# Kernel optimization log

Hardware: AMD Instinct MI355X
Metric: run time of the kernel (lower is better)

The kernel has to match this reference:

```python
import jax, jax.numpy as jnp
import numpy as np


def setup_inputs() -> dict:
    key = jax.random.key(0)
    k1, k2, k3, k4 = jax.random.split(key, 4)
    n, m = 4096, 1024  # n video frames, 1024-d features
    scale = 0.02
    return {
        "x": jax.random.normal(k1, (n, m), dtype=jnp.float32),
        "WQ": jax.random.normal(k2, (m, m), dtype=jnp.float32) * scale,  # torch Linear weight [out,in]
        "WK": jax.random.normal(k3, (m, m), dtype=jnp.float32) * scale,
        "WV": jax.random.normal(k4, (m, m), dtype=jnp.float32) * scale,
    }


def _quaternion_logits(q, k):
    """Hamilton-product attention logits: 4 tensors of shape [Lq, Lk]."""
    qr, qx, qy, qz = jnp.split(q, 4, axis=-1)
    kr, kx, ky, kz = jnp.split(k, 4, axis=-1)
    dot = lambda a, b: jnp.einsum('qd,kd->qk', a, b)
    r = dot(qr, kr) - dot(qx, kx) - dot(qy, ky) - dot(qz, kz)
    i = dot(qr, kx) + dot(qx, kr) + dot(qy, kz) - dot(qz, ky)
    j = dot(qr, ky) - dot(qx, kz) + dot(qy, kr) + dot(qz, kx)
    kk = dot(qr, kz) + dot(qx, ky) - dot(qy, kx) + dot(qz, kr)
    return [r, i, j, kk]


def reference(x, WQ, WK, WV):
    # QKV projections (torch Linear, no bias): y = x @ W.T
    Q = x @ WQ.T
    K = x @ WK.T
    V = x @ WV.T
    v_vals = jnp.split(V, 4, axis=-1)  # 4 chunks of depth d/4 (tensor2tensor quaternion attn)
    logits = _quaternion_logits(Q, K)
    outs = []
    w = None
    for l, v in zip(logits, v_vals):
        w = jax.nn.softmax(l, axis=-1)  # per-component softmax over keys
        outs.append(w @ v)
    y = jnp.concatenate(outs, axis=-1)  # [n, d]
    # original returns the attention weights from the last component (loop-leaked var)
    return y, w
```

## Files before the change

kernel.cpp:

```cpp
#include <hip/hip_runtime.h>
#include <cmath>

typedef __attribute__((ext_vector_type(8))) short short8;
typedef __attribute__((ext_vector_type(8))) unsigned short ushort8_t;
typedef __attribute__((ext_vector_type(8))) _Float16 half8;
typedef __attribute__((ext_vector_type(4))) float f32x4;
typedef unsigned short u16;

__device__ __forceinline__ u16 f2h(float f) {
    _Float16 h = (_Float16)f;
    return __builtin_bit_cast(u16, h);
}
__device__ __forceinline__ float h2f(u16 b) {
    return (float)__builtin_bit_cast(_Float16, b);
}

#define GLD16(g, l)                                                              \
    __builtin_amdgcn_global_load_lds(                                            \
        (const __attribute__((address_space(1))) unsigned int*)(g),              \
        (__attribute__((address_space(3))) unsigned int*)(l), 16, 0, 0)

#define MFMA_F16(a, b, c)                                                        \
    __builtin_amdgcn_mfma_f32_16x16x32_f16(                                      \
        __builtin_bit_cast(half8, (a)), __builtin_bit_cast(half8, (b)), (c), 0, 0, 0)
#define SBAR() asm volatile("s_barrier" ::: "memory")

__global__ __launch_bounds__(256) void to_h_all(
    const float* __restrict__ x, const float* __restrict__ WQ,
    const float* __restrict__ WK, const float* __restrict__ WV,
    u16* __restrict__ xh, u16* __restrict__ Wh)
{
    int bid = blockIdx.x;
    const float* src;
    u16* dst;
    int off;
    if (bid < 4096) { src = x; dst = xh; off = bid; }
    else {
        int j = bid - 4096;
        int wsel = j >> 10;
        off = j & 1023;
        src = wsel == 0 ? WQ : (wsel == 1 ? WK : WV);
        dst = Wh + (size_t)wsel * 1024 * 1024;
    }
    int idx = off * 256 + threadIdx.x;
    float4 v = reinterpret_cast<const float4*>(src)[idx];
    ushort4 h;
    h.x = f2h(v.x); h.y = f2h(v.y); h.z = f2h(v.z); h.w = f2h(v.w);
    reinterpret_cast<ushort4*>(dst)[idx] = h;
}

__global__ __launch_bounds__(512, 2) void logits8(
    const u16* __restrict__ A, const u16* __restrict__ B, const u16* __restrict__ Bneg,
    u16* __restrict__ Pbase, float* __restrict__ pmb, float* __restrict__ psb,
    int perm_all, int sign_all)
{
    constexpr int NT = 16;
    __shared__ u16 L[2][2][256 * 64];
    const int tid = threadIdx.x;
    const int l = tid & 63, w = tid >> 6;
    const int wr = w >> 2, wc = w & 3;
    const int lr = l & 15, lh = l >> 4;
    const int bid = (int)blockIdx.x;
    const int comp = bid >> 8;
    const int perm_packed = (perm_all >> (8 * comp)) & 0xFF;
    const int sign_packed = (sign_all >> (8 * comp)) & 0xFF;
    u16* P = Pbase + (size_t)comp * 4096 * 4096;
    float* pm = pmb + (size_t)comp * 4096 * 64;
    float* ps = psb + (size_t)comp * 4096 * 64;
    const int inner = bid & 255;
    const int xcd = inner & 7, idx = inner >> 3;
    const int rowp = (xcd >> 1) * 4 + (idx >> 3);
    const int colp = (xcd & 1) * 8 + (idx & 7);
    const int row0 = rowp * 256, col0 = colp * 256;
    const int srow = l >> 3;
    const int scol = ((l & 7) ^ (l >> 3)) * 8;

    f32x4 acc[8][4] = {};

    auto stage = [&](int t) {
        int kA = t * 64;
        int ch = kA >> 8;
        int p = (perm_packed >> (2 * ch)) & 3;
        const u16* Bsrc = ((sign_packed >> ch) & 1) ? Bneg : B;
        int kB = (p << 8) + (kA & 255);
        int bf = t & 1;
        #pragma unroll
        for (int i = 0; i < 4; ++i) {
            int r0 = w * 32 + i * 8;
            GLD16(&A[(size_t)(row0 + r0 + srow) * 1024 + kA + scol], &L[bf][0][r0 * 64]);
        }
        #pragma unroll
        for (int i = 0; i < 4; ++i) {
            int r0 = w * 32 + i * 8;
            GLD16(&Bsrc[(size_t)(col0 + r0 + srow) * 1024 + kB + scol], &L[bf][1][r0 * 64]);
        }
    };
    auto readA = [&](int bf, int m, int kh) -> short8 {
        int row = wr * 128 + m * 16 + lr;
        int c = ((kh * 4 + lh) ^ (lr & 7)) * 8;
        return *reinterpret_cast<const short8*>(&L[bf][0][row * 64 + c]);
    };
    auto readB = [&](int bf, int n, int kh) -> short8 {
        int row = wc * 64 + n * 16 + lr;
        int c = ((kh * 4 + lh) ^ (lr & 7)) * 8;
        return *reinterpret_cast<const short8*>(&L[bf][1][row * 64 + c]);
    };

    stage(0);
    stage(1);
    asm volatile("s_waitcnt vmcnt(8)" ::: "memory");
    SBAR();

    #pragma unroll 2
    for (int t = 0; t < NT; ++t) {
        const int bf = t & 1;
        short8 am[4][2], bn[4][2];
        #pragma unroll
        for (int m = 0; m < 4; ++m) { am[m][0] = readA(bf, m, 0); am[m][1] = readA(bf, m, 1); }
        #pragma unroll
        for (int n = 0; n < 2; ++n) { bn[n][0] = readB(bf, n, 0); bn[n][1] = readB(bf, n, 1); }
        SBAR();
        __builtin_amdgcn_s_setprio(1);
        #pragma unroll
        for (int m = 0; m < 4; ++m)
            #pragma unroll
            for (int n = 0; n < 2; ++n) {
                acc[m][n] = MFMA_F16(am[m][0], bn[n][0], acc[m][n]);
                acc[m][n] = MFMA_F16(am[m][1], bn[n][1], acc[m][n]);
            }
        __builtin_amdgcn_s_setprio(0);
        SBAR();
        #pragma unroll
        for (int n = 2; n < 4; ++n) { bn[n][0] = readB(bf, n, 0); bn[n][1] = readB(bf, n, 1); }
        SBAR();
        __builtin_amdgcn_s_setprio(1);
        #pragma unroll
        for (int m = 0; m < 4; ++m)
            #pragma unroll
            for (int n = 2; n < 4; ++n) {
                acc[m][n] = MFMA_F16(am[m][0], bn[n][0], acc[m][n]);
                acc[m][n] = MFMA_F16(am[m][1], bn[n][1], acc[m][n]);
            }
        __builtin_amdgcn_s_setprio(0);
        SBAR();
        #pragma unroll
        for (int m = 0; m < 4; ++m) { am[m][0] = readA(bf, 4 + m, 0); am[m][1] = readA(bf, 4 + m, 1); }
        SBAR();
        __builtin_amdgcn_s_setprio(1);
        #pragma unroll
        for (int m = 0; m < 4; ++m)
            #pragma unroll
            for (int n = 2; n < 4; ++n) {
                acc[4 + m][n] = MFMA_F16(am[m][0], bn[n][0], acc[4 + m][n]);
                acc[4 + m][n] = MFMA_F16(am[m][1], bn[n][1], acc[4 + m][n]);
            }
        __builtin_amdgcn_s_setprio(0);
        SBAR();
        if (t + 2 < NT) stage(t + 2);
        SBAR();
        __builtin_amdgcn_s_setprio(1);
        #pragma unroll
        for (int m = 0; m < 4; ++m)
            #pragma unroll
            for (int n = 0; n < 2; ++n) {
                acc[4 + m][n] = MFMA_F16(am[m][0], bn[n][0], acc[4 + m][n]);
                acc[4 + m][n] = MFMA_F16(am[m][1], bn[n][1], acc[4 + m][n]);
            }
        __builtin_amdgcn_s_setprio(0);
        if (t + 2 < NT) { asm volatile("s_waitcnt vmcnt(8)" ::: "memory"); }
        else           { asm volatile("s_waitcnt vmcnt(0)" ::: "memory"); }
        SBAR();
    }

    const int tcol = (col0 >> 6) + wc;
    float* T = reinterpret_cast<float*>(&L[0][0][0]) + w * 1088;
    const int rq = l >> 2;
    const int cq = l & 3;
    #pragma unroll
    for (int m = 0; m < 8; ++m) {
        #pragma unroll
        for (int n = 0; n < 4; ++n)
            #pragma unroll
            for (int j = 0; j < 4; ++j)
                T[(lh * 4 + j) * 68 + n * 16 + lr] = acc[m][n][j];
        float vals[16];
        #pragma unroll
        for (int q = 0; q < 4; ++q) {
            f32x4 v4 = *reinterpret_cast<const f32x4*>(&T[rq * 68 + cq * 16 + q * 4]);
            vals[q * 4 + 0] = v4[0]; vals[q * 4 + 1] = v4[1];
            vals[q * 4 + 2] = v4[2]; vals[q * 4 + 3] = v4[3];
        }
        float mx = vals[0];
        #pragma unroll
        for (int c = 1; c < 16; ++c) mx = fmaxf(mx, vals[c]);
        mx = fmaxf(mx, __shfl_xor(mx, 1, 64));
        mx = fmaxf(mx, __shfl_xor(mx, 2, 64));
        float e[16];
        float s = 0.f;
        #pragma unroll
        for (int c = 0; c < 16; ++c) { e[c] = expf(vals[c] - mx); s += e[c]; }
        s += __shfl_xor(s, 1, 64);
        s += __shfl_xor(s, 2, 64);
        int row = row0 + wr * 128 + m * 16 + rq;
        if (cq == 0) {
            pm[(size_t)row * 64 + tcol] = mx;
            ps[(size_t)row * 64 + tcol] = s;
        }
        ushort8_t d0, d1;
        #pragma unroll
        for (int c = 0; c < 8; ++c) d0[c] = f2h(e[c]);
        #pragma unroll
        for (int c = 0; c < 8; ++c) d1[c] = f2h(e[c + 8]);
        size_t go = (size_t)row * 4096 + col0 + wc * 64 + cq * 16;
        *reinterpret_cast<ushort8_t*>(&P[go]) = d0;
        *reinterpret_cast<ushort8_t*>(&P[go + 8]) = d1;
    }
}

__global__ __launch_bounds__(512, 2) void qkv8(
    const u16* __restrict__ A, const u16* __restrict__ B,
    u16* __restrict__ Qh, u16* __restrict__ Kh, u16* __restrict__ Khn,
    u16* __restrict__ Vt)
{
    constexpr int NT = 16;
    __shared__ u16 L[2][2][256 * 64];
    const int tid = threadIdx.x;
    const int l = tid & 63, w = tid >> 6;
    const int wr = w >> 2, wc = w & 3;
    const int lr = l & 15, lh = l >> 4;
    const int bid = (int)blockIdx.x;
    const int wgid = (bid & 7) * 24 + (bid >> 3);
    const int row0 = (wgid / 12) * 256, col0 = (wgid % 12) * 256;
    const int srow = l >> 3;
    const int scol = ((l & 7) ^ (l >> 3)) * 8;

    f32x4 acc[8][4] = {};

    auto stage = [&](int t) {
        int k0 = t * 64;
        int bf = t & 1;
        #pragma unroll
        for (int i = 0; i < 4; ++i) {
            int r0 = w * 32 + i * 8;
            GLD16(&A[(size_t)(row0 + r0 + srow) * 1024 + k0 + scol], &L[bf][0][r0 * 64]);
        }
        #pragma unroll
        for (int i = 0; i < 4; ++i) {
            int r0 = w * 32 + i * 8;
            GLD16(&B[(size_t)(col0 + r0 + srow) * 1024 + k0 + scol], &L[bf][1][r0 * 64]);
        }
    };
    auto readA = [&](int bf, int m, int kh) -> short8 {
        int row = wr * 128 + m * 16 + lr;
        int c = ((kh * 4 + lh) ^ (lr & 7)) * 8;
        return *reinterpret_cast<const short8*>(&L[bf][0][row * 64 + c]);
    };
    auto readB = [&](int bf, int n, int kh) -> short8 {
        int row = wc * 64 + n * 16 + lr;
        int c = ((kh * 4 + lh) ^ (lr & 7)) * 8;
        return *reinterpret_cast<const short8*>(&L[bf][1][row * 64 + c]);
    };

    stage(0);
    stage(1);
    asm volatile("s_waitcnt vmcnt(8)" ::: "memory");
    SBAR();

    #pragma unroll 2
    for (int t = 0; t < NT; ++t) {
        const int bf = t & 1;
        short8 am[4][2], bn[4][2];
        #pragma unroll
        for (int m = 0; m < 4; ++m) { am[m][0] = readA(bf, m, 0); am[m][1] = readA(bf, m, 1); }
        #pragma unroll
        for (int n = 0; n < 2; ++n) { bn[n][0] = readB(bf, n, 0); bn[n][1] = readB(bf, n, 1); }
        SBAR();
        __builtin_amdgcn_s_setprio(1);
        #pragma unroll
        for (int m = 0; m < 4; ++m)
            #pragma unroll
            for (int n = 0; n < 2; ++n) {
                acc[m][n] = MFMA_F16(am[m][0], bn[n][0], acc[m][n]);
                acc[m][n] = MFMA_F16(am[m][1], bn[n][1], acc[m][n]);
            }
        __builtin_amdgcn_s_setprio(0);
        SBAR();
        #pragma unroll
        for (int n = 2; n < 4; ++n) { bn[n][0] = readB(bf, n, 0); bn[n][1] = readB(bf, n, 1); }
        SBAR();
        __builtin_amdgcn_s_setprio(1);
        #pragma unroll
        for (int m = 0; m < 4; ++m)
            #pragma unroll
            for (int n = 2; n < 4; ++n) {
                acc[m][n] = MFMA_F16(am[m][0], bn[n][0], acc[m][n]);
                acc[m][n] = MFMA_F16(am[m][1], bn[n][1], acc[m][n]);
            }
        __builtin_amdgcn_s_setprio(0);
        SBAR();
        #pragma unroll
        for (int m = 0; m < 4; ++m) { am[m][0] = readA(bf, 4 + m, 0); am[m][1] = readA(bf, 4 + m, 1); }
        SBAR();
        __builtin_amdgcn_s_setprio(1);
        #pragma unroll
        for (int m = 0; m < 4; ++m)
            #pragma unroll
            for (int n = 2; n < 4; ++n) {
                acc[4 + m][n] = MFMA_F16(am[m][0], bn[n][0], acc[4 + m][n]);
                acc[4 + m][n] = MFMA_F16(am[m][1], bn[n][1], acc[4 + m][n]);
            }
        __builtin_amdgcn_s_setprio(0);
        SBAR();
        if (t + 2 < NT) stage(t + 2);
        SBAR();
        __builtin_amdgcn_s_setprio(1);
        #pragma unroll
        for (int m = 0; m < 4; ++m)
            #pragma unroll
            for (int n = 0; n < 2; ++n) {
                acc[4 + m][n] = MFMA_F16(am[m][0], bn[n][0], acc[4 + m][n]);
                acc[4 + m][n] = MFMA_F16(am[m][1], bn[n][1], acc[4 + m][n]);
            }
        __builtin_amdgcn_s_setprio(0);
        if (t + 2 < NT) { asm volatile("s_waitcnt vmcnt(8)" ::: "memory"); }
        else           { asm volatile("s_waitcnt vmcnt(0)" ::: "memory"); }
        SBAR();
    }

    const int mode = col0 >> 10;
    #pragma unroll
    for (int m = 0; m < 8; ++m)
        #pragma unroll
        for (int n = 0; n < 4; ++n) {
            int gr = row0 + wr * 128 + m * 16 + lh * 4;
            int gc = col0 + wc * 64 + n * 16 + lr;
            int gcl = gc & 1023;
            f32x4 v = acc[m][n];
            if (mode == 0) {
                #pragma unroll
                for (int j = 0; j < 4; ++j)
                    Qh[(size_t)(gr + j) * 1024 + gcl] = f2h(v[j]);
            } else if (mode == 1) {
                #pragma unroll
                for (int j = 0; j < 4; ++j) {
                    u16 h = f2h(v[j]);
                    size_t o = (size_t)(gr + j) * 1024 + gcl;
                    Kh[o] = h; Khn[o] = h ^ 0x8000;
                }
            } else {
                ushort4 o;
                o.x = f2h(v[0]); o.y = f2h(v[1]); o.z = f2h(v[2]); o.w = f2h(v[3]);
                *reinterpret_cast<ushort4*>(&Vt[(size_t)gcl * 4096 + gr]) = o;
            }
        }
}

template<bool WRITE_W>
__global__ __launch_bounds__(256) void pv_fused(
    const u16* __restrict__ P, float* __restrict__ Wout,
    const u16* __restrict__ Vt, const float* __restrict__ pm,
    const float* __restrict__ ps, u16* __restrict__ ypart, int c256)
{
    __shared__ u16 As[64 * 64];
    __shared__ u16 Bs[256 * 64];
    __shared__ float Red[64][4];
    __shared__ float Ms[64], Is[64];
    const int tid = threadIdx.x;
    const int l = tid & 63, w = tid >> 6;
    const int lr = l & 15, lh = l >> 4;
    const int kc = blockIdx.x;
    const int row0 = blockIdx.y * 64;
    const int kbase = kc * 512;
    const int srow = l >> 3, scol = ((l & 7) ^ (l >> 3)) * 8;

    {
        int row = tid & 63, part = tid >> 6;
        const float* pmr = &pm[(size_t)(row0 + row) * 64 + part * 16];
        const float* psr = &ps[(size_t)(row0 + row) * 64 + part * 16];
        float M = -INFINITY;
        #pragma unroll
        for (int i = 0; i < 16; ++i) M = fmaxf(M, pmr[i]);
        Red[row][part] = M;
        __syncthreads();
        float Mg = fmaxf(fmaxf(Red[row][0], Red[row][1]),
                         fmaxf(Red[row][2], Red[row][3]));
        float S = 0.f;
        #pragma unroll
        for (int i = 0; i < 16; ++i) S += psr[i] * expf(pmr[i] - Mg);
        __syncthreads();
        Red[row][part] = S;
        __syncthreads();
        if (tid < 64) {
            float Sg = Red[tid][0] + Red[tid][1] + Red[tid][2] + Red[tid][3];
            Ms[tid] = Mg;
            Is[tid] = 1.0f / Sg;
        }
        __syncthreads();
    }

    float Mr[4], Ir[4];
    #pragma unroll
    for (int i = 0; i < 4; ++i) { int r = (tid >> 4) + i * 16; Mr[i] = Ms[r]; Ir[i] = Is[r]; }

    f32x4 acc[4][4] = {};

    for (int kt = 0; kt < 8; ++kt) {
        const int tcol = kc * 8 + kt;
        __syncthreads();
        #pragma unroll
        for (int i = 0; i < 4; ++i) {
            int idx = tid + i * 256;
            int r = idx >> 4, s4 = idx & 15;
            float alpha = expf(pm[(size_t)(row0 + r) * 64 + tcol] - Mr[i]) * Ir[i];
            size_t ga = (size_t)(row0 + r) * 4096 + kbase + kt * 64 + s4 * 4;
            ushort4 dv = *reinterpret_cast<const ushort4*>(&P[ga]);
            float e0 = h2f(dv.x) * alpha;
            float e1 = h2f(dv.y) * alpha;
            float e2 = h2f(dv.z) * alpha;
            float e3 = h2f(dv.w) * alpha;
            if (WRITE_W)
                *reinterpret_cast<float4*>(&Wout[ga]) = make_float4(e0, e1, e2, e3);
            ushort4 h;
            h.x = f2h(e0); h.y = f2h(e1); h.z = f2h(e2); h.w = f2h(e3);
            int dst = ((s4 >> 1) ^ (r & 7)) * 8 + (s4 & 1) * 4;
            *reinterpret_cast<ushort4*>(&As[r * 64 + dst]) = h;
        }
        #pragma unroll
        for (int i = 0; i < 8; ++i) {
            int r0 = w * 64 + i * 8;
            GLD16(&Vt[(size_t)(c256 + r0 + srow) * 4096 + kbase + kt * 64 + scol],
                  &Bs[r0 * 64]);
        }
        __syncthreads();
        #pragma unroll
        for (int kh = 0; kh < 2; ++kh) {
            short8 af[4], bfv[4];
            #pragma unroll
            for (int m = 0; m < 4; ++m)
                af[m] = *reinterpret_cast<const short8*>(
                    &As[(m * 16 + lr) * 64 + ((kh * 4 + lh) ^ (lr & 7)) * 8]);
            #pragma unroll
            for (int n = 0; n < 4; ++n)
                bfv[n] = *reinterpret_cast<const short8*>(
                    &Bs[(w * 64 + n * 16 + lr) * 64 + ((kh * 4 + lh) ^ (lr & 7)) * 8]);
            #pragma unroll
            for (int m = 0; m < 4; ++m)
                #pragma unroll
                for (int n = 0; n < 4; ++n)
                    acc[m][n] = MFMA_F16(af[m], bfv[n], acc[m][n]);
        }
    }

    #pragma unroll
    for (int m = 0; m < 4; ++m)
        #pragma unroll
        for (int n = 0; n < 4; ++n) {
            int rr = m * 16 + lh * 4;
            int col = w * 64 + n * 16 + lr;
            #pragma unroll
            for (int j = 0; j < 4; ++j)
                ypart[((size_t)kc * 4096 + row0 + rr + j) * 256 + col] = f2h(acc[m][n][j]);
        }
}

__global__ __launch_bounds__(256) void reduce_y(const u16* __restrict__ ypart,
                                                float* __restrict__ y, int c256)
{
    int idx = blockIdx.x * 256 + threadIdx.x;
    int r = idx >> 6, c4 = (idx & 63) * 4;
    float s0 = 0.f, s1 = 0.f, s2 = 0.f, s3 = 0.f;
    #pragma unroll
    for (int kc = 0; kc < 8; ++kc) {
        ushort4 p = *reinterpret_cast<const ushort4*>(
            &ypart[((size_t)kc * 4096 + r) * 256 + c4]);
        s0 += h2f(p.x); s1 += h2f(p.y); s2 += h2f(p.z); s3 += h2f(p.w);
    }
    *reinterpret_cast<float4*>(&y[(size_t)r * 1024 + c256 + c4]) =
        make_float4(s0, s1, s2, s3);
}

extern "C" void kernel_launch(void* const* d_in, const int* in_sizes, int n_in,
                              void* d_out, int out_size, void* d_ws, size_t ws_size,
                              hipStream_t stream)
{
    const int n = 4096, d = 1024;
    const size_t NN = (size_t)n * n;
    const float* x  = (const float*)d_in[0];
    const float* WQ = (const float*)d_in[1];
    const float* WK = (const float*)d_in[2];
    const float* WV = (const float*)d_in[3];

    float* y = (float*)d_out;
    float* wout = y + (size_t)n * d;

    const int permv[4] = {0xE4, 0xB1, 0x4E, 0x1B};
    const int signv[4] = {0x0E, 0x08, 0x02, 0x04};
    const int PERM_ALL = 0x1B4EB1E4;
    const int SIGN_ALL = 0x0402080E;

    const size_t need_mega =
        (4 * NN + 4 * (size_t)n * d + (size_t)8 * n * 256) * 2 +
        2 * 4 * (size_t)n * 64 * 4;

    if (ws_size >= need_mega) {
        u16* P4   = (u16*)d_ws;
        u16* xh   = P4;
        u16* Wh   = P4 + (size_t)n * 1024;
        u16* Qh   = P4 + 4 * NN;
        u16* Kh   = Qh + (size_t)n * 1024;
        u16* Khn  = Kh + (size_t)n * 1024;
        u16* Vt   = Khn + (size_t)n * 1024;
        u16* ypart = Vt + (size_t)d * 4096;
        float* pm4 = (float*)(ypart + (size_t)8 * n * 256);
        float* ps4 = pm4 + 4 * (size_t)n * 64;

        to_h_all<<<7168, 256, 0, stream>>>(x, WQ, WK, WV, xh, Wh);
        qkv8<<<192, 512, 0, stream>>>(xh, Wh, Qh, Kh, Khn, Vt);
        logits8<<<1024, 512, 0, stream>>>(Qh, Kh, Khn, P4, pm4, ps4,
                                          PERM_ALL, SIGN_ALL);
        for (int c = 0; c < 4; ++c) {
            const u16* Pc = P4 + (size_t)c * NN;
            const float* pmc = pm4 + (size_t)c * n * 64;
            const float* psc = ps4 + (size_t)c * n * 64;
            if (c == 3)
                pv_fused<true><<<dim3(8, 64), 256, 0, stream>>>(
                    Pc, wout, Vt, pmc, psc, ypart, c * 256);
            else
                pv_fused<false><<<dim3(8, 64), 256, 0, stream>>>(
                    Pc, wout, Vt, pmc, psc, ypart, c * 256);
            reduce_y<<<1024, 256, 0, stream>>>(ypart, y, c * 256);
        }
    } else {
        u16* P    = (u16*)d_ws;
        u16* xh   = P;
        u16* Wh   = P + (size_t)n * 1024;
        u16* Qh   = P + NN;
        u16* Kh   = Qh + (size_t)n * 1024;
        u16* Khn  = Kh + (size_t)n * 1024;
        u16* Vt   = Khn + (size_t)n * 1024;
        u16* ypart = Vt + (size_t)d * 4096;
        float* pm = (float*)(ypart + (size_t)8 * n * 256);
        float* ps = pm + (size_t)n * 64;

        to_h_all<<<7168, 256, 0, stream>>>(x, WQ, WK, WV, xh, Wh);
        qkv8<<<192, 512, 0, stream>>>(xh, Wh, Qh, Kh, Khn, Vt);
        for (int c = 0; c < 4; ++c) {
            logits8<<<256, 512, 0, stream>>>(Qh, Kh, Khn, P, pm, ps,
                                             permv[c], signv[c]);
            if (c == 3)
                pv_fused<true><<<dim3(8, 64), 256, 0, stream>>>(
                    P, wout, Vt, pm, ps, ypart, c * 256);
            else
                pv_fused<false><<<dim3(8, 64), 256, 0, stream>>>(
                    P, wout, Vt, pm, ps, ypart, c * 256);
            reduce_y<<<1024, 256, 0, stream>>>(ypart, y, c * 256);
        }
    }
}
```

Before: 330.3 us.

## Halve logits K-tile to shrink LDS and batch y reductions into one launch

The logits GEMM now stages 32-wide K slices instead of 64 and runs twice as many iterations, with a 4-way swizzle in place of the 8-way one. This halves the LDS footprint per block, which may let more blocks share a CU, at the cost of more barriers per unit of work. Separately, each component's partial outputs go to their own buffer, and the four per-component reduce launches become a single reduce4 launch. The fallback path for small workspaces is removed, so the code now assumes the larger workspace is available.

```diff
diff --git a/kernel.cpp b/kernel.cpp
--- a/kernel.cpp
+++ b/kernel.cpp
@@ -54,8 +54,8 @@
     u16* __restrict__ Pbase, float* __restrict__ pmb, float* __restrict__ psb,
     int perm_all, int sign_all)
 {
-    constexpr int NT = 16;
-    __shared__ u16 L[2][2][256 * 64];
+    constexpr int NT = 32;
+    __shared__ u16 L[2][2][256 * 32];
     const int tid = threadIdx.x;
     const int l = tid & 63, w = tid >> 6;
     const int wr = w >> 2, wc = w & 3;
@@ -72,88 +72,82 @@
     const int rowp = (xcd >> 1) * 4 + (idx >> 3);
     const int colp = (xcd & 1) * 8 + (idx & 7);
     const int row0 = rowp * 256, col0 = colp * 256;
-    const int srow = l >> 3;
-    const int scol = ((l & 7) ^ (l >> 3)) * 8;
+    const int srow = l >> 2;
+    const int scol = (((l & 3) ^ (srow & 3))) * 8;
 
     f32x4 acc[8][4] = {};
 
     auto stage = [&](int t) {
-        int kA = t * 64;
+        int kA = t * 32;
         int ch = kA >> 8;
         int p = (perm_packed >> (2 * ch)) & 3;
         const u16* Bsrc = ((sign_packed >> ch) & 1) ? Bneg : B;
         int kB = (p << 8) + (kA & 255);
         int bf = t & 1;
         #pragma unroll
-        for (int i = 0; i < 4; ++i) {
-            int r0 = w * 32 + i * 8;
-            GLD16(&A[(size_t)(row0 + r0 + srow) * 1024 + kA + scol], &L[bf][0][r0 * 64]);
-        }
-        #pragma unroll
-        for (int i = 0; i < 4; ++i) {
-            int r0 = w * 32 + i * 8;
-            GLD16(&Bsrc[(size_t)(col0 + r0 + srow) * 1024 + kB + scol], &L[bf][1][r0 * 64]);
+        for (int i = 0; i < 2; ++i) {
+            int r0 = w * 32 + i * 16;
+            GLD16(&A[(size_t)(row0 + r0 + srow) * 1024 + kA + scol], &L[bf][0][r0 * 32]);
+        }
+        #pragma unroll
+        for (int i = 0; i < 2; ++i) {
+            int r0 = w * 32 + i * 16;
+            GLD16(&Bsrc[(size_t)(col0 + r0 + srow) * 1024 + kB + scol], &L[bf][1][r0 * 32]);
         }
     };
-    auto readA = [&](int bf, int m, int kh) -> short8 {
+    auto readA = [&](int bf, int m) -> short8 {
         int row = wr * 128 + m * 16 + lr;
-        int c = ((kh * 4 + lh) ^ (lr & 7)) * 8;
-        return *reinterpret_cast<const short8*>(&L[bf][0][row * 64 + c]);
+        int c = (lh ^ (lr & 3)) * 8;
+        return *reinterpret_cast<const short8*>(&L[bf][0][row * 32 + c]);
     };
-    auto readB = [&](int bf, int n, int kh) -> short8 {
+    auto readB = [&](int bf, int n) -> short8 {
         int row = wc * 64 + n * 16 + lr;
-        int c = ((kh * 4 + lh) ^ (lr & 7)) * 8;
-        return *reinterpret_cast<const short8*>(&L[bf][1][row * 64 + c]);
+        int c = (lh ^ (lr & 3)) * 8;
+        return *reinterpret_cast<const short8*>(&L[bf][1][row * 32 + c]);
     };
 
     stage(0);
     stage(1);
-    asm volatile("s_waitcnt vmcnt(8)" ::: "memory");
+    asm volatile("s_waitcnt vmcnt(4)" ::: "memory");
     SBAR();
 
     #pragma unroll 2
     for (int t = 0; t < NT; ++t) {
         const int bf = t & 1;
-        short8 am[4][2], bn[4][2];
-        #pragma unroll
-        for (int m = 0; m < 4; ++m) { am[m][0] = readA(bf, m, 0); am[m][1] = readA(bf, m, 1); }
-        #pragma unroll
-        for (int n = 0; n < 2; ++n) { bn[n][0] = readB(bf, n, 0); bn[n][1] = readB(bf, n, 1); }
-        SBAR();
-        __builtin_amdgcn_s_setprio(1);
-        #pragma unroll
-        for (int m = 0; m < 4; ++m)
-            #pragma unroll
-            for (int n = 0; n < 2; ++n) {
-                acc[m][n] = MFMA_F16(am[m][0], bn[n][0], acc[m][n]);
-                acc[m][n] = MFMA_F16(am[m][1], bn[n][1], acc[m][n]);
-            }
-        __builtin_amdgcn_s_setprio(0);
-        SBAR();
-        #pragma unroll
-        for (int n = 2; n < 4; ++n) { bn[n][0] = readB(bf, n, 0); bn[n][1] = readB(bf, n, 1); }
-        SBAR();
-        __builtin_amdgcn_s_setprio(1);
-        #pragma unroll
-        for (int m = 0; m < 4; ++m)
-            #pragma unroll
-            for (int n = 2; n < 4; ++n) {
-                acc[m][n] = MFMA_F16(am[m][0], bn[n][0], acc[m][n]);
-                acc[m][n] = MFMA_F16(am[m][1], bn[n][1], acc[m][n]);
-            }
-        __builtin_amdgcn_s_setprio(0);
-        SBAR();
-        #pragma unroll
-        for (int m = 0; m < 4; ++m) { am[m][0] = readA(bf, 4 + m, 0); am[m][1] = readA(bf, 4 + m, 1); }
-        SBAR();
-        __builtin_amdgcn_s_setprio(1);
-        #pragma unroll
-        for (int m = 0; m < 4; ++m)
-            #pragma unroll
-            for (int n = 2; n < 4; ++n) {
-                acc[4 + m][n] = MFMA_F16(am[m][0], bn[n][0], acc[4 + m][n]);
-                acc[4 + m][n] = MFMA_F16(am[m][1], bn[n][1], acc[4 + m][n]);
-            }
+        short8 am[4], bn[4];
+        #pragma unroll
+        for (int m = 0; m < 4; ++m) am[m] = readA(bf, m);
+        #pragma unroll
+        for (int n = 0; n < 2; ++n) bn[n] = readB(bf, n);
+        SBAR();
+        __builtin_amdgcn_s_setprio(1);
+        #pragma unroll
+        for (int m = 0; m < 4; ++m)
+            #pragma unroll
+            for (int n = 0; n < 2; ++n)
+                acc[m][n] = MFMA_F16(am[m], bn[n], acc[m][n]);
+        __builtin_amdgcn_s_setprio(0);
+        SBAR();
+        #pragma unroll
+        for (int n = 2; n < 4; ++n) bn[n] = readB(bf, n);
+        SBAR();
+        __builtin_amdgcn_s_setprio(1);
+        #pragma unroll
+        for (int m = 0; m < 4; ++m)
+            #pragma unroll
+            for (int n = 2; n < 4; ++n)
+                acc[m][n] = MFMA_F16(am[m], bn[n], acc[m][n]);
+        __builtin_amdgcn_s_setprio(0);
+        SBAR();
+        #pragma unroll
+        for (int m = 0; m < 4; ++m) am[m] = readA(bf, 4 + m);
+        SBAR();
+        __builtin_amdgcn_s_setprio(1);
+        #pragma unroll
+        for (int m = 0; m < 4; ++m)
+            #pragma unroll
+            for (int n = 2; n < 4; ++n)
+                acc[4 + m][n] = MFMA_F16(am[m], bn[n], acc[4 + m][n]);
         __builtin_amdgcn_s_setprio(0);
         SBAR();
         if (t + 2 < NT) stage(t + 2);
@@ -162,12 +156,10 @@
         #pragma unroll
         for (int m = 0; m < 4; ++m)
             #pragma unroll
-            for (int n = 0; n < 2; ++n) {
-                acc[4 + m][n] = MFMA_F16(am[m][0], bn[n][0], acc[4 + m][n]);
-                acc[4 + m][n] = MFMA_F16(am[m][1], bn[n][1], acc[4 + m][n]);
-            }
-        __builtin_amdgcn_s_setprio(0);
-        if (t + 2 < NT) { asm volatile("s_waitcnt vmcnt(8)" ::: "memory"); }
+            for (int n = 0; n < 2; ++n)
+                acc[4 + m][n] = MFMA_F16(am[m], bn[n], acc[4 + m][n]);
+        __builtin_amdgcn_s_setprio(0);
+        if (t + 2 < NT) { asm volatile("s_waitcnt vmcnt(4)" ::: "memory"); }
         else           { asm volatile("s_waitcnt vmcnt(0)" ::: "memory"); }
         SBAR();
     }
@@ -463,10 +455,13 @@
         }
 }
 
-__global__ __launch_bounds__(256) void reduce_y(const u16* __restrict__ ypart,
-                                                float* __restrict__ y, int c256)
+__global__ __launch_bounds__(256) void reduce4(const u16* __restrict__ ypart4,
+                                               float* __restrict__ y)
 {
-    int idx = blockIdx.x * 256 + threadIdx.x;
+    int bid = blockIdx.x;
+    int comp = bid >> 10;
+    int idx = (bid & 1023) * 256 + threadIdx.x;
+    const u16* ypart = ypart4 + (size_t)comp * 8 * 4096 * 256;
     int r = idx >> 6, c4 = (idx & 63) * 4;
     float s0 = 0.f, s1 = 0.f, s2 = 0.f, s3 = 0.f;
     #pragma unroll
@@ -475,7 +470,7 @@
             &ypart[((size_t)kc * 4096 + r) * 256 + c4]);
         s0 += h2f(p.x); s1 += h2f(p.y); s2 += h2f(p.z); s3 += h2f(p.w);
     }
-    *reinterpret_cast<float4*>(&y[(size_t)r * 1024 + c256 + c4]) =
+    *reinterpret_cast<float4*>(&y[(size_t)r * 1024 + comp * 256 + c4]) =
         make_float4(s0, s1, s2, s3);
 }
 
@@ -493,67 +488,37 @@
     float* y = (float*)d_out;
     float* wout = y + (size_t)n * d;
 
-    const int permv[4] = {0xE4, 0xB1, 0x4E, 0x1B};
-    const int signv[4] = {0x0E, 0x08, 0x02, 0x04};
     const int PERM_ALL = 0x1B4EB1E4;
     const int SIGN_ALL = 0x0402080E;
 
-    const size_t need_mega =
-        (4 * NN + 4 * (size_t)n * d + (size_t)8 * n * 256) * 2 +
-        2 * 4 * (size_t)n * 64 * 4;
-
-    if (ws_size >= need_mega) {
-        u16* P4   = (u16*)d_ws;
-        u16* xh   = P4;
-        u16* Wh   = P4 + (size_t)n * 1024;
-        u16* Qh   = P4 + 4 * NN;
-        u16* Kh   = Qh + (size_t)n * 1024;
-        u16* Khn  = Kh + (size_t)n * 1024;
-        u16* Vt   = Khn + (size_t)n * 1024;
-        u16* ypart = Vt + (size_t)d * 4096;
-        float* pm4 = (float*)(ypart + (size_t)8 * n * 256);
-        float* ps4 = pm4 + 4 * (size_t)n * 64;
-
-        to_h_all<<<7168, 256, 0, stream>>>(x, WQ, WK, WV, xh, Wh);
-        qkv8<<<192, 512, 0, stream>>>(xh, Wh, Qh, Kh, Khn, Vt);
-        logits8<<<1024, 512, 0, stream>>>(Qh, Kh, Khn, P4, pm4, ps4,
-                                          PERM_ALL, SIGN_ALL);
-        for (int c = 0; c < 4; ++c) {
-            const u16* Pc = P4 + (size_t)c * NN;
-            const float* pmc = pm4 + (size_t)c * n * 64;
-            const float* psc = ps4 + (size_t)c * n * 64;
-            if (c == 3)
-                pv_fused<true><<<dim3(8, 64), 256, 0, stream>>>(
-                    Pc, wout, Vt, pmc, psc, ypart, c * 256);
-            else
-                pv_fused<false><<<dim3(8, 64), 256, 0, stream>>>(
-                    Pc, wout, Vt, pmc, psc, ypart, c * 256);
-            reduce_y<<<1024, 256, 0, stream>>>(ypart, y, c * 256);
-        }
-    } else {
-        u16* P    = (u16*)d_ws;
-        u16* xh   = P;
-        u16* Wh   = P + (size_t)n * 1024;
-        u16* Qh   = P + NN;
-        u16* Kh   = Qh + (size_t)n * 1024;
-        u16* Khn  = Kh + (size_t)n * 1024;
-        u16* Vt   = Khn + (size_t)n * 1024;
-        u16* ypart = Vt + (size_t)d * 4096;
-        float* pm = (float*)(ypart + (size_t)8 * n * 256);
-        float* ps = pm + (size_t)n * 64;
-
-        to_h_all<<<7168, 256, 0, stream>>>(x, WQ, WK, WV, xh, Wh);
-        qkv8<<<192, 512, 0, stream>>>(xh, Wh, Qh, Kh, Khn, Vt);
-        for (int c = 0; c < 4; ++c) {
-            logits8<<<256, 512, 0, stream>>>(Qh, Kh, Khn, P, pm, ps,
-                                             permv[c], signv[c]);
-            if (c == 3)
-                pv_fused<true><<<dim3(8, 64), 256, 0, stream>>>(
-                    P, wout, Vt, pm, ps, ypart, c * 256);
-            else
-                pv_fused<false><<<dim3(8, 64), 256, 0, stream>>>(
-                    P, wout, Vt, pm, ps, ypart, c * 256);
-            reduce_y<<<1024, 256, 0, stream>>>(ypart, y, c * 256);
-        }
-    }
-}
+    const size_t ypart_sz = (size_t)8 * n * 256;
+
+    u16* P4   = (u16*)d_ws;
+    u16* xh   = P4;
+    u16* Wh   = P4 + (size_t)n * 1024;
+    u16* Qh   = P4 + 4 * NN;
+    u16* Kh   = Qh + (size_t)n * 1024;
+    u16* Khn  = Kh + (size_t)n * 1024;
+    u16* Vt   = Khn + (size_t)n * 1024;
+    u16* ypart4 = Vt + (size_t)d * 4096;
+    float* pm4 = (float*)(ypart4 + 4 * ypart_sz);
+    float* ps4 = pm4 + 4 * (size_t)n * 64;
+
+    to_h_all<<<7168, 256, 0, stream>>>(x, WQ, WK, WV, xh, Wh);
+    qkv8<<<192, 512, 0, stream>>>(xh, Wh, Qh, Kh, Khn, Vt);
+    logits8<<<1024, 512, 0, stream>>>(Qh, Kh, Khn, P4, pm4, ps4,
+                                      PERM_ALL, SIGN_ALL);
+    for (int c = 0; c < 4; ++c) {
+        const u16* Pc = P4 + (size_t)c * NN;
+        const float* pmc = pm4 + (size_t)c * n * 64;
+        const float* psc = ps4 + (size_t)c * n * 64;
+        u16* yp = ypart4 + (size_t)c * ypart_sz;
+        if (c == 3)
+            pv_fused<true><<<dim3(8, 64), 256, 0, stream>>>(
+                Pc, wout, Vt, pmc, psc, yp, c * 256);
+        else
+            pv_fused<false><<<dim3(8, 64), 256, 0, stream>>>(
+                Pc, wout, Vt, pmc, psc, yp, c * 256);
+    }
+    reduce4<<<4096, 256, 0, stream>>>(ypart4, y);
+}
```

Measured after the change: 344.9 us. 1.04x slower.
